# Kernel tuning notes

Hardware: AMD Instinct MI355X
Metric: run time of the kernel (lower is better)

The kernel has to match this reference:

```python
import jax, jax.numpy as jnp
import numpy as np


def setup_inputs() -> dict:
    key = jax.random.key(0)
    k1, k2 = jax.random.split(key)
    B, D, C = 4096, 128, 64
    score = jax.random.normal(k1, (B, D), dtype=jnp.float32)
    target = jax.random.randint(k2, (B,), 0, C, dtype=jnp.int64)
    alpha = jnp.full((1,), 9.0, dtype=jnp.float32)  # learned margin param
    return {"score": score, "target": target, "alpha": alpha}


def _pairwise_dist(score):
    # squared euclidean: ||xi||^2 + ||xj||^2 - 2 xi.xj, clamped at 0, then sqrt
    mag = jnp.sum(score * score, axis=1)            # [B]
    d2 = mag[:, None] + mag[None, :] - 2.0 * (score @ score.T)
    d2 = jnp.maximum(d2, 0.0)
    # safe sqrt (diagonal is exactly 0; avoid nan grads)
    safe = jnp.where(d2 > 0.0, d2, 1.0)
    return jnp.where(d2 > 0.0, jnp.sqrt(safe), 0.0)  # [B, B]


def reference(score, target, alpha):
    target = target.reshape(-1)
    B = score.shape[0]
    dist = _pairwise_dist(score)                    # [B, B]
    diff = target[:, None] != target[None, :]       # [B, B] negative-pair mask
    # per-anchor sum over negatives of exp(alpha - dist); diagonal excluded (same label)
    nes = jnp.sum(jnp.where(diff, jnp.exp(alpha[0] - dist), 0.0), axis=1)  # [B]
    l_n = jnp.log(nes[:, None] + nes[None, :])      # [B, B]
    # positive pairs i<j with equal labels
    upper = jnp.triu(jnp.ones((B, B), dtype=bool), k=1)
    pos = (~diff) & upper
    terms = jnp.where(pos, jax.nn.relu(l_n + dist) ** 2, 0.0)
    counter = jnp.sum(pos).astype(score.dtype)
    return jnp.sum(terms) / (2.0 * counter)
```

## Files before the change

### kernel.cpp

```cpp
#include <hip/hip_runtime.h>
#include <math.h>

#define BN 4096
#define DD 128
#define NCLS 64
#define NT 32
#define NTILE2 (NT * NT)
#define NJB 32
#define SLOTS 2048
#define OVCAP (8u * 1024u * 1024u)

typedef __attribute__((ext_vector_type(8))) short short8;
typedef __attribute__((ext_vector_type(4))) float f32x4;

__device__ __forceinline__ unsigned short f2bf(float f) {
    unsigned int u = __float_as_uint(f);
    u += 0x7FFFu + ((u >> 16) & 1u);
    return (unsigned short)(u >> 16);
}


__global__ __launch_bounds__(256)
void prep_kernel(const float* __restrict__ score, unsigned short* __restrict__ sbf,
                 float* __restrict__ mag) {
    int row  = blockIdx.x * 4 + (threadIdx.x >> 6);
    int lane = threadIdx.x & 63;
    float2 v = *reinterpret_cast<const float2*>(score + (size_t)row * DD + lane * 2);
    float s = v.x * v.x + v.y * v.y;
    #pragma unroll
    for (int off = 32; off; off >>= 1) s += __shfl_xor(s, off);
    ushort2 u; u.x = f2bf(v.x); u.y = f2bf(v.y);
    *reinterpret_cast<ushort2*>(sbf + (size_t)row * DD + lane * 2) = u;
    if (lane == 0) mag[row] = s;
}

__global__ __launch_bounds__(256)
void nes_kernel(const unsigned short* __restrict__ sbf, const int* __restrict__ target,
                const float* __restrict__ alphap, const float* __restrict__ mag,
                float* __restrict__ nes_part,
                uint2* __restrict__ recs, uint2* __restrict__ ovrecs,
                int* __restrict__ tilecnt, unsigned int* __restrict__ ovcnt) {
    const int ib = blockIdx.x, jb = blockIdx.y;
    const int tile = ib * NT + jb;
    if (jb < ib) {
        if (threadIdx.x == 0) tilecnt[tile] = 0;
        return;
    }
    __shared__ float rowsum[2][128];
    __shared__ float colsum[2][128];
    __shared__ int lcnt;
    const int tid = threadIdx.x;
    const int w = tid >> 6, lane = tid & 63;
    const int lhi = lane >> 4, llo = lane & 15;
    const int i0 = ib * 128, j0 = jb * 128;
    const bool diag = (ib == jb);
    const int wr = w >> 1, wc = w & 1;

    if (tid == 0) lcnt = 0;
    __syncthreads();

    f32x4 acc[4][4] = {};
    #pragma unroll
    for (int kk = 0; kk < 4; ++kk) {
        short8 a[4], b[4];
        #pragma unroll
        for (int m = 0; m < 4; ++m) {
            int r = i0 + wr * 64 + m * 16 + llo;
            a[m] = *reinterpret_cast<const short8*>(sbf + (size_t)r * DD + kk * 32 + lhi * 8);
        }
        #pragma unroll
        for (int n = 0; n < 4; ++n) {
            int r = j0 + wc * 64 + n * 16 + llo;
            b[n] = *reinterpret_cast<const short8*>(sbf + (size_t)r * DD + kk * 32 + lhi * 8);
        }
        #pragma unroll
        for (int m = 0; m < 4; ++m)
            #pragma unroll
            for (int n = 0; n < 4; ++n)
                acc[m][n] = __builtin_amdgcn_mfma_f32_16x16x32_bf16(a[m], b[n], acc[m][n], 0, 0, 0);
    }

    const float alpha = alphap[0];
    float mj[4]; int tj[4]; int jj[4];
    #pragma unroll
    for (int n = 0; n < 4; ++n) {
        int j = j0 + wc * 64 + n * 16 + llo;
        jj[n] = j; mj[n] = mag[j]; tj[n] = target[j];
    }
    float cs[4] = {0.f, 0.f, 0.f, 0.f};
    #pragma unroll
    for (int m = 0; m < 4; ++m) {
        #pragma unroll
        for (int rg = 0; rg < 4; ++rg) {
            int li = wr * 64 + m * 16 + lhi * 4 + rg;
            int i = i0 + li;
            float mi = mag[i];
            int ti = target[i];
            float rs = 0.f;
            #pragma unroll
            for (int n = 0; n < 4; ++n) {
                float d2 = fmaxf(mi + mj[n] - 2.0f * acc[m][n][rg], 0.0f);
                float dist = sqrtf(d2);
                bool p = (ti == tj[n]);
                float e = p ? 0.0f : __expf(alpha - dist);
                rs += e;
                cs[n] += e;
                if (p && jj[n] > i) {
                    int slot = atomicAdd(&lcnt, 1);
                    uint2 r;
                    r.x = __float_as_uint(dist);
                    r.y = ((unsigned)i << 16) | (unsigned)jj[n];
                    if (slot < SLOTS) recs[(size_t)tile * SLOTS + slot] = r;
                    else {
                        unsigned o = atomicAdd(ovcnt, 1u);
                        if (o < OVCAP) ovrecs[o] = r;
                    }
                }
            }
            rs += __shfl_xor(rs, 1);
            rs += __shfl_xor(rs, 2);
            rs += __shfl_xor(rs, 4);
            rs += __shfl_xor(rs, 8);
            if (llo == 0) rowsum[wc][li] = rs;
        }
    }
    #pragma unroll
    for (int n = 0; n < 4; ++n) {
        cs[n] += __shfl_xor(cs[n], 16);
        cs[n] += __shfl_xor(cs[n], 32);
        if (lhi == 0) colsum[wr][wc * 64 + n * 16 + llo] = cs[n];
    }
    __syncthreads();
    if (tid < 128) {
        nes_part[(size_t)jb * BN + i0 + tid] = rowsum[0][tid] + rowsum[1][tid];
        if (!diag)
            nes_part[(size_t)ib * BN + j0 + tid] = colsum[0][tid] + colsum[1][tid];
    }
    if (tid == 0) tilecnt[tile] = lcnt;
}

__global__ __launch_bounds__(256)
void nes_reduce_kernel(const float* __restrict__ nes_part, float* __restrict__ nes) {
    int t = blockIdx.x * 256 + threadIdx.x;
    float s = 0.f;
    #pragma unroll
    for (int k = 0; k < NJB; ++k) s += nes_part[(size_t)k * BN + t];
    nes[t] = s;
}

__global__ __launch_bounds__(256)
void pos_kernel(const uint2* __restrict__ recs, const uint2* __restrict__ ovrecs,
                const int* __restrict__ tilecnt, const unsigned int* __restrict__ ovcnt,
                const float* __restrict__ nes,
                float* __restrict__ part_sum, unsigned int* __restrict__ part_cnt) {
    __shared__ float ssum[4];
    __shared__ unsigned int scnt[4];
    const int t = blockIdx.x;
    const int tid = threadIdx.x;
    const int w = tid >> 6;
    int cnt = tilecnt[t];
    if (cnt > SLOTS) cnt = SLOTS;
    float s = 0.f;
    unsigned int cc = 0;
    for (int k = tid; k < cnt; k += 256) {
        uint2 r = recs[(size_t)t * SLOTS + k];
        float dist = __uint_as_float(r.x);
        int i = r.y >> 16, j = r.y & 0xFFFF;
        float tv = __logf(nes[i] + nes[j]) + dist;
        if (tv > 0.f) s += tv * tv;
        cc++;
    }
    unsigned int oc = *ovcnt;
    if (oc > OVCAP) oc = OVCAP;
    for (unsigned int k = (unsigned)t * 256u + tid; k < oc; k += NTILE2 * 256u) {
        uint2 r = ovrecs[k];
        float dist = __uint_as_float(r.x);
        int i = r.y >> 16, j = r.y & 0xFFFF;
        float tv = __logf(nes[i] + nes[j]) + dist;
        if (tv > 0.f) s += tv * tv;
        cc++;
    }
    #pragma unroll
    for (int off = 1; off < 64; off <<= 1) {
        s += __shfl_xor(s, off);
        cc += __shfl_xor(cc, off);
    }
    if ((tid & 63) == 0) { ssum[w] = s; scnt[w] = cc; }
    __syncthreads();
    if (tid == 0) {
        part_sum[t] = ssum[0] + ssum[1] + ssum[2] + ssum[3];
        part_cnt[t] = scnt[0] + scnt[1] + scnt[2] + scnt[3];
    }
}

__global__ __launch_bounds__(256)
void finalize_kernel(const float* __restrict__ part_sum,
                     const unsigned int* __restrict__ part_cnt,
                     float* __restrict__ out) {
    __shared__ float fs[4];
    __shared__ unsigned int fc[4];
    int tid = threadIdx.x;
    float s = 0.f;
    unsigned int c = 0;
    #pragma unroll
    for (int k = 0; k < NTILE2 / 256; ++k) {
        s += part_sum[k * 256 + tid];
        c += part_cnt[k * 256 + tid];
    }
    #pragma unroll
    for (int off = 1; off < 64; off <<= 1) {
        s += __shfl_xor(s, off);
        c += __shfl_xor(c, off);
    }
    if ((tid & 63) == 0) { fs[tid >> 6] = s; fc[tid >> 6] = c; }
    __syncthreads();
    if (tid == 0) {
        float S = fs[0] + fs[1] + fs[2] + fs[3];
        float C = (float)(fc[0] + fc[1] + fc[2] + fc[3]);
        out[0] = S / (2.0f * C);
    }
}

extern "C" void kernel_launch(void* const* d_in, const int* in_sizes, int n_in,
                              void* d_out, int out_size, void* d_ws, size_t ws_size,
                              hipStream_t stream) {
    const float* score  = (const float*)d_in[0];
    const int*   target = (const int*)d_in[1];
    const float* alpha  = (const float*)d_in[2];
    float* out = (float*)d_out;

    unsigned short* sbf = (unsigned short*)d_ws;
    float* mag      = (float*)((char*)d_ws + (size_t)BN * DD * 2);
    float* nes_part = mag + BN;
    float* nes      = nes_part + (size_t)NJB * BN;
    float* part_sum = nes + BN;
    unsigned int* part_cnt = (unsigned int*)(part_sum + NTILE2);
    int* tilecnt    = (int*)(part_cnt + NTILE2);
    unsigned int* ovcnt = (unsigned int*)(tilecnt + NTILE2);
    uint2* recs     = (uint2*)(ovcnt + 16);
    uint2* ovrecs   = recs + (size_t)NTILE2 * SLOTS;

    hipMemsetAsync(ovcnt, 0, sizeof(unsigned int), stream);

    prep_kernel<<<BN / 4, 256, 0, stream>>>(score, sbf, mag);
    dim3 g(NT, NT);
    nes_kernel<<<g, 256, 0, stream>>>(sbf, target, alpha, mag, nes_part,
                                      recs, ovrecs, tilecnt, ovcnt);
    nes_reduce_kernel<<<BN / 256, 256, 0, stream>>>(nes_part, nes);
    pos_kernel<<<NTILE2, 256, 0, stream>>>(recs, ovrecs, tilecnt, ovcnt, nes,
                                           part_sum, part_cnt);
    finalize_kernel<<<1, 256, 0, stream>>>(part_sum, part_cnt, out);
}
```

Before: 111.8 us.

## Assign one 64x64 upper-triangle tile per wavefront with ballot-based record compaction

Replaces the 32x32 block grid, where half the blocks exit immediately, with a packed upper-triangular list of 64x64 tiles, each handled by a single wavefront. Shared-memory row/column sums, block barriers and the LDS atomic counter go away: sums are written directly to nes_part, and positive-pair records are compacted with ballot/popcount. Each wave preloads all its A/B fragments into registers before the MFMA loop. The trade-offs are higher register pressure, a serial loop to decode the tile index, more pos_kernel blocks, and a wider partial-sum reduction (64 slices).

```diff
diff --git a/kernel.cpp b/kernel.cpp
--- a/kernel.cpp
+++ b/kernel.cpp
@@ -3,12 +3,11 @@
 
 #define BN 4096
 #define DD 128
-#define NCLS 64
-#define NT 32
-#define NTILE2 (NT * NT)
-#define NJB 32
-#define SLOTS 2048
-#define OVCAP (8u * 1024u * 1024u)
+#define NWT 64
+#define NTILES (NWT * (NWT + 1) / 2)
+#define NJB 64
+#define SLOTS 1024
+#define OVCAP (4u * 1024u * 1024u)
 
 typedef __attribute__((ext_vector_type(8))) short short8;
 typedef __attribute__((ext_vector_type(4))) float f32x4;
@@ -40,60 +39,55 @@
                 float* __restrict__ nes_part,
                 uint2* __restrict__ recs, uint2* __restrict__ ovrecs,
                 int* __restrict__ tilecnt, unsigned int* __restrict__ ovcnt) {
-    const int ib = blockIdx.x, jb = blockIdx.y;
-    const int tile = ib * NT + jb;
-    if (jb < ib) {
-        if (threadIdx.x == 0) tilecnt[tile] = 0;
-        return;
-    }
-    __shared__ float rowsum[2][128];
-    __shared__ float colsum[2][128];
-    __shared__ int lcnt;
     const int tid = threadIdx.x;
     const int w = tid >> 6, lane = tid & 63;
     const int lhi = lane >> 4, llo = lane & 15;
-    const int i0 = ib * 128, j0 = jb * 128;
+    const int t = blockIdx.x * 4 + w;
+    if (t >= NTILES) return;
+
+    int ib = 0, rem = t, rl = NWT;
+    while (rem >= rl) { rem -= rl; ++ib; --rl; }
+    const int jb = ib + rem;
+    const int i0 = ib * 64, j0 = jb * 64;
     const bool diag = (ib == jb);
-    const int wr = w >> 1, wc = w & 1;
-
-    if (tid == 0) lcnt = 0;
-    __syncthreads();
+
+    short8 a[4][4], b[4][4];
+    #pragma unroll
+    for (int m = 0; m < 4; ++m)
+        #pragma unroll
+        for (int kk = 0; kk < 4; ++kk)
+            a[m][kk] = *reinterpret_cast<const short8*>(
+                sbf + (size_t)(i0 + m * 16 + llo) * DD + kk * 32 + lhi * 8);
+    #pragma unroll
+    for (int n = 0; n < 4; ++n)
+        #pragma unroll
+        for (int kk = 0; kk < 4; ++kk)
+            b[n][kk] = *reinterpret_cast<const short8*>(
+                sbf + (size_t)(j0 + n * 16 + llo) * DD + kk * 32 + lhi * 8);
 
     f32x4 acc[4][4] = {};
     #pragma unroll
-    for (int kk = 0; kk < 4; ++kk) {
-        short8 a[4], b[4];
-        #pragma unroll
-        for (int m = 0; m < 4; ++m) {
-            int r = i0 + wr * 64 + m * 16 + llo;
-            a[m] = *reinterpret_cast<const short8*>(sbf + (size_t)r * DD + kk * 32 + lhi * 8);
-        }
-        #pragma unroll
-        for (int n = 0; n < 4; ++n) {
-            int r = j0 + wc * 64 + n * 16 + llo;
-            b[n] = *reinterpret_cast<const short8*>(sbf + (size_t)r * DD + kk * 32 + lhi * 8);
-        }
+    for (int kk = 0; kk < 4; ++kk)
         #pragma unroll
         for (int m = 0; m < 4; ++m)
             #pragma unroll
             for (int n = 0; n < 4; ++n)
-                acc[m][n] = __builtin_amdgcn_mfma_f32_16x16x32_bf16(a[m], b[n], acc[m][n], 0, 0, 0);
-    }
+                acc[m][n] = __builtin_amdgcn_mfma_f32_16x16x32_bf16(a[m][kk], b[n][kk], acc[m][n], 0, 0, 0);
 
     const float alpha = alphap[0];
     float mj[4]; int tj[4]; int jj[4];
     #pragma unroll
     for (int n = 0; n < 4; ++n) {
-        int j = j0 + wc * 64 + n * 16 + llo;
+        int j = j0 + n * 16 + llo;
         jj[n] = j; mj[n] = mag[j]; tj[n] = target[j];
     }
     float cs[4] = {0.f, 0.f, 0.f, 0.f};
+    unsigned int wbase = 0;
     #pragma unroll
     for (int m = 0; m < 4; ++m) {
         #pragma unroll
         for (int rg = 0; rg < 4; ++rg) {
-            int li = wr * 64 + m * 16 + lhi * 4 + rg;
-            int i = i0 + li;
+            int i = i0 + m * 16 + lhi * 4 + rg;
             float mi = mag[i];
             int ti = target[i];
             float rs = 0.f;
@@ -105,38 +99,37 @@
                 float e = p ? 0.0f : __expf(alpha - dist);
                 rs += e;
                 cs[n] += e;
-                if (p && jj[n] > i) {
-                    int slot = atomicAdd(&lcnt, 1);
+                bool emit = p && (jj[n] > i);
+                unsigned long long mask = __ballot(emit);
+                if (emit) {
+                    unsigned pos = (unsigned)__popcll(mask & ((1ULL << lane) - 1ULL));
+                    unsigned slot = wbase + pos;
                     uint2 r;
                     r.x = __float_as_uint(dist);
                     r.y = ((unsigned)i << 16) | (unsigned)jj[n];
-                    if (slot < SLOTS) recs[(size_t)tile * SLOTS + slot] = r;
+                    if (slot < SLOTS) recs[(size_t)t * SLOTS + slot] = r;
                     else {
                         unsigned o = atomicAdd(ovcnt, 1u);
                         if (o < OVCAP) ovrecs[o] = r;
                     }
                 }
+                wbase += (unsigned)__popcll(mask);
             }
             rs += __shfl_xor(rs, 1);
             rs += __shfl_xor(rs, 2);
             rs += __shfl_xor(rs, 4);
             rs += __shfl_xor(rs, 8);
-            if (llo == 0) rowsum[wc][li] = rs;
+            if (llo == 0) nes_part[(size_t)jb * BN + i] = rs;
         }
     }
     #pragma unroll
     for (int n = 0; n < 4; ++n) {
         cs[n] += __shfl_xor(cs[n], 16);
         cs[n] += __shfl_xor(cs[n], 32);
-        if (lhi == 0) colsum[wr][wc * 64 + n * 16 + llo] = cs[n];
-    }
-    __syncthreads();
-    if (tid < 128) {
-        nes_part[(size_t)jb * BN + i0 + tid] = rowsum[0][tid] + rowsum[1][tid];
-        if (!diag)
-            nes_part[(size_t)ib * BN + j0 + tid] = colsum[0][tid] + colsum[1][tid];
-    }
-    if (tid == 0) tilecnt[tile] = lcnt;
+        if (!diag && lane < 16)
+            nes_part[(size_t)ib * BN + jj[n]] = cs[n];
+    }
+    if (lane == 0) tilecnt[t] = (int)wbase;
 }
 
 __global__ __launch_bounds__(256)
@@ -172,7 +165,7 @@
     }
     unsigned int oc = *ovcnt;
     if (oc > OVCAP) oc = OVCAP;
-    for (unsigned int k = (unsigned)t * 256u + tid; k < oc; k += NTILE2 * 256u) {
+    for (unsigned int k = (unsigned)t * 256u + tid; k < oc; k += (unsigned)NTILES * 256u) {
         uint2 r = ovrecs[k];
         float dist = __uint_as_float(r.x);
         int i = r.y >> 16, j = r.y & 0xFFFF;
@@ -203,9 +196,12 @@
     float s = 0.f;
     unsigned int c = 0;
     #pragma unroll
-    for (int k = 0; k < NTILE2 / 256; ++k) {
-        s += part_sum[k * 256 + tid];
-        c += part_cnt[k * 256 + tid];
+    for (int k = 0; k < 9; ++k) {
+        int idx = k * 256 + tid;
+        if (idx < NTILES) {
+            s += part_sum[idx];
+            c += part_cnt[idx];
+        }
     }
     #pragma unroll
     for (int off = 1; off < 64; off <<= 1) {
@@ -234,20 +230,19 @@
     float* nes_part = mag + BN;
     float* nes      = nes_part + (size_t)NJB * BN;
     float* part_sum = nes + BN;
-    unsigned int* part_cnt = (unsigned int*)(part_sum + NTILE2);
-    int* tilecnt    = (int*)(part_cnt + NTILE2);
-    unsigned int* ovcnt = (unsigned int*)(tilecnt + NTILE2);
+    unsigned int* part_cnt = (unsigned int*)(part_sum + NTILES);
+    int* tilecnt    = (int*)(part_cnt + NTILES);
+    unsigned int* ovcnt = (unsigned int*)(tilecnt + NTILES);
     uint2* recs     = (uint2*)(ovcnt + 16);
-    uint2* ovrecs   = recs + (size_t)NTILE2 * SLOTS;
+    uint2* ovrecs   = recs + (size_t)NTILES * SLOTS;
 
     hipMemsetAsync(ovcnt, 0, sizeof(unsigned int), stream);
 
     prep_kernel<<<BN / 4, 256, 0, stream>>>(score, sbf, mag);
-    dim3 g(NT, NT);
-    nes_kernel<<<g, 256, 0, stream>>>(sbf, target, alpha, mag, nes_part,
-                                      recs, ovrecs, tilecnt, ovcnt);
+    nes_kernel<<<(NTILES + 3) / 4, 256, 0, stream>>>(sbf, target, alpha, mag, nes_part,
+                                                     recs, ovrecs, tilecnt, ovcnt);
     nes_reduce_kernel<<<BN / 256, 256, 0, stream>>>(nes_part, nes);
-    pos_kernel<<<NTILE2, 256, 0, stream>>>(recs, ovrecs, tilecnt, ovcnt, nes,
+    pos_kernel<<<NTILES, 256, 0, stream>>>(recs, ovrecs, tilecnt, ovcnt, nes,
                                            part_sum, part_cnt);
     finalize_kernel<<<1, 256, 0, stream>>>(part_sum, part_cnt, out);
 }
```

Measured after the change: 127.3 us. 1.14x slower.
